# Kernel optimization log

Hardware: AMD Instinct MI355X
Metric: run time of the kernel (lower is better)

Reference implementation:

```python
import jax, jax.numpy as jnp
import numpy as np

B, S, DM, H = 8, 1024, 256, 8
D = DM // H  # 32


def setup_inputs() -> dict:
    key = jax.random.key(0)
    ks = jax.random.split(key, 8)
    xav = (6.0 / (DM + DM)) ** 0.5  # xavier_uniform bound for square Linear
    return {
        "q": jax.random.normal(ks[0], (B, S, DM), jnp.float32),
        "k": jax.random.normal(ks[1], (B, S, DM), jnp.float32),
        "v": jax.random.normal(ks[2], (B, S, DM), jnp.float32),
        "mask": jnp.tril(jnp.ones((1, 1, S, S), jnp.int32)),  # causal: mask==0 is disallowed
        "zero_pad": 1,
        "k_index": 5,
        "Wk": jax.random.uniform(ks[3], (DM, DM), jnp.float32, -xav, xav),
        "bk": jnp.zeros((DM,), jnp.float32),
        "Wv": jax.random.uniform(ks[4], (DM, DM), jnp.float32, -xav, xav),
        "bv": jnp.zeros((DM,), jnp.float32),
        "Wo": jax.random.uniform(ks[5], (DM, DM), jnp.float32, -xav, xav),
        "bo": jnp.zeros((DM,), jnp.float32),
    }


def _attention4sparse_kt(qh, kh, vh, mask, zero_pad, k_index):
    # qh/kh/vh: [B,H,S,D]; mask: [1,1,S,S]
    d = qh.shape[-1]
    scores = jnp.einsum("bhid,bhjd->bhij", qh, kh) / jnp.sqrt(jnp.float32(d))
    scores = jnp.where(mask == 0, jnp.float32(-1e32), scores)
    attn = jax.nn.softmax(scores, axis=-1)  # [B,H,S,S]
    seqlen = attn.shape[2]
    if k_index + 1 < seqlen:
        # per-row k_index-th largest prob as threshold; keep top-k_index entries, re-softmax
        thresh = jax.lax.top_k(attn, k_index)[0][..., -1:]  # [B,H,S,1]
        sparse = jnp.where(attn - thresh >= 0.0, attn, jnp.float32(-1e16))
        resoft = jax.nn.softmax(sparse, axis=-1)
        rows = jnp.arange(seqlen)[None, None, :, None]
        # rows 0..k_index keep the original softmax; later rows use sparsified re-softmax
        attn = jnp.where(rows <= k_index, attn, resoft)
    if zero_pad:
        attn = attn.at[:, :, 0, :].set(0.0)
    out = jnp.einsum("bhij,bhjd->bhid", attn, vh)
    return out, attn


def reference(q, k, v, mask, zero_pad, k_index, Wk, bk, Wv, bv, Wo, bo):
    bs = q.shape[0]
    # key_query_same=True: q and k share k_linear
    kh = (k @ Wk.T + bk).reshape(bs, -1, H, D).transpose(0, 2, 1, 3)
    qh = (q @ Wk.T + bk).reshape(bs, -1, H, D).transpose(0, 2, 1, 3)
    vh = (v @ Wv.T + bv).reshape(bs, -1, H, D).transpose(0, 2, 1, 3)
    out, attn = _attention4sparse_kt(qh, kh, vh, mask, zero_pad, k_index)
    concat = out.transpose(0, 2, 1, 3).reshape(bs, -1, DM)
    output = concat @ Wo.T + bo
    return output, attn
```

## Files before the change

### kernel.cpp

```cpp
#include <hip/hip_runtime.h>
#include <cfloat>
#include <cmath>

#define S_LEN  1024
#define DHEAD  32
#define NHEAD  8
#define DMODEL 256

__global__ __launch_bounds__(256)
void proj_gemm(const float* __restrict__ q, const float* __restrict__ k, const float* __restrict__ v,
               const float* __restrict__ Wk, const float* __restrict__ bk,
               const float* __restrict__ Wv, const float* __restrict__ bv,
               float* __restrict__ qh, float* __restrict__ kh, float* __restrict__ vh)
{
    __shared__ float Xs[128*36];
    __shared__ float Ws_[128*36];
    const int z = blockIdx.z;
    const float* X    = (z==0) ? q  : ((z==1) ? k  : v);
    const float* W    = (z==2) ? Wv : Wk;
    const float* bias = (z==2) ? bv : bk;
    float*       C    = (z==0) ? qh : ((z==1) ? kh : vh);

    const int tid  = threadIdx.x;
    const int row0 = blockIdx.x * 128;
    const int col0 = blockIdx.y * 128;
    const int tx = tid & 15, ty = tid >> 4;
    const int sr = tid >> 1, shf = tid & 1;

    float acc[8][8];
    #pragma unroll
    for (int a = 0; a < 8; ++a)
        #pragma unroll
        for (int b = 0; b < 8; ++b) acc[a][b] = 0.f;

    const int xg = ty & 7;
    const int wg = tx & 7;
    const int swb = (sr >> 3) & 7;

    for (int k0 = 0; k0 < DMODEL; k0 += 32) {
        const float4* xp = (const float4*)(X + (size_t)(row0 + sr) * DMODEL + k0 + shf*16);
        const float4* wp = (const float4*)(W + (size_t)(col0 + sr) * DMODEL + k0 + shf*16);
        float4 xv[4], wv[4];
        #pragma unroll
        for (int q4 = 0; q4 < 4; ++q4) { xv[q4] = xp[q4]; wv[q4] = wp[q4]; }
        if (k0) __syncthreads();
        #pragma unroll
        for (int q4 = 0; q4 < 4; ++q4) {
            const int slot = (shf*4 + q4) ^ swb;
            *(float4*)&Xs [sr*36 + slot*4] = xv[q4];
            *(float4*)&Ws_[sr*36 + slot*4] = wv[q4];
        }
        __syncthreads();
        #pragma unroll
        for (int g = 0; g < 8; ++g) {
            float4 xf[8];
            #pragma unroll
            for (int ri = 0; ri < 8; ++ri)
                xf[ri] = *(const float4*)&Xs[(ty*8+ri)*36 + ((g ^ xg) << 2)];
            #pragma unroll
            for (int ci = 0; ci < 8; ++ci) {
                const float4 wf = *(const float4*)&Ws_[(tx*8+ci)*36 + ((g ^ wg) << 2)];
                #pragma unroll
                for (int ri = 0; ri < 8; ++ri) {
                    acc[ri][ci] += xf[ri].x * wf.x;
                    acc[ri][ci] += xf[ri].y * wf.y;
                    acc[ri][ci] += xf[ri].z * wf.z;
                    acc[ri][ci] += xf[ri].w * wf.w;
                }
            }
        }
    }

    #pragma unroll
    for (int ri = 0; ri < 8; ++ri) {
        const int r = row0 + ty*8 + ri;
        const int bI = r >> 10, s = r & 1023;
        #pragma unroll
        for (int half = 0; half < 2; ++half) {
            const int c = col0 + tx*8 + half*4;
            const float4 bv4 = *(const float4*)(bias + c);
            float4 o;
            o.x = acc[ri][half*4+0] + bv4.x;
            o.y = acc[ri][half*4+1] + bv4.y;
            o.z = acc[ri][half*4+2] + bv4.z;
            o.w = acc[ri][half*4+3] + bv4.w;
            const int h = c >> 5, d0 = c & 31;
            *(float4*)(C + (((size_t)(bI*NHEAD + h))*S_LEN + s)*DHEAD + d0) = o;
        }
    }
}

__global__ __launch_bounds__(256)
void out_gemm(const float* __restrict__ X, const float* __restrict__ W,
              const float* __restrict__ bias, float* __restrict__ C)
{
    __shared__ float Xs[128*36];
    __shared__ float Ws_[64*36];
    const int tid  = threadIdx.x;
    const int row0 = blockIdx.x * 128;
    const int col0 = blockIdx.y * 64;
    const int tx = tid & 15, ty = tid >> 4;
    const int sr = tid >> 1, shf = tid & 1;
    const int wc = tid >> 2, wq = tid & 3;

    float acc[8][4];
    #pragma unroll
    for (int a = 0; a < 8; ++a)
        #pragma unroll
        for (int b = 0; b < 4; ++b) acc[a][b] = 0.f;

    const int xg  = ty & 7;
    const int wg2 = (tx >> 1) & 7;
    const int swbx = (sr >> 3) & 7;
    const int swbw = (wc >> 3) & 7;

    for (int k0 = 0; k0 < DMODEL; k0 += 32) {
        const float4* xp = (const float4*)(X + (size_t)(row0 + sr) * DMODEL + k0 + shf*16);
        const float4* wp = (const float4*)(W + (size_t)(col0 + wc) * DMODEL + k0 + wq*8);
        float4 xv[4], wv[2];
        #pragma unroll
        for (int q4 = 0; q4 < 4; ++q4) xv[q4] = xp[q4];
        #pragma unroll
        for (int q2 = 0; q2 < 2; ++q2) wv[q2] = wp[q2];
        if (k0) __syncthreads();
        #pragma unroll
        for (int q4 = 0; q4 < 4; ++q4) {
            const int slot = (shf*4 + q4) ^ swbx;
            *(float4*)&Xs[sr*36 + slot*4] = xv[q4];
        }
        #pragma unroll
        for (int q2 = 0; q2 < 2; ++q2) {
            const int slot = (wq*2 + q2) ^ swbw;
            *(float4*)&Ws_[wc*36 + slot*4] = wv[q2];
        }
        __syncthreads();
        #pragma unroll
        for (int g = 0; g < 8; ++g) {
            float4 xf[8];
            #pragma unroll
            for (int ri = 0; ri < 8; ++ri)
                xf[ri] = *(const float4*)&Xs[(ty*8+ri)*36 + ((g ^ xg) << 2)];
            #pragma unroll
            for (int ci = 0; ci < 4; ++ci) {
                const float4 wf = *(const float4*)&Ws_[(tx*4+ci)*36 + ((g ^ wg2) << 2)];
                #pragma unroll
                for (int ri = 0; ri < 8; ++ri) {
                    acc[ri][ci] += xf[ri].x * wf.x;
                    acc[ri][ci] += xf[ri].y * wf.y;
                    acc[ri][ci] += xf[ri].z * wf.z;
                    acc[ri][ci] += xf[ri].w * wf.w;
                }
            }
        }
    }

    #pragma unroll
    for (int ri = 0; ri < 8; ++ri) {
        const int r = row0 + ty*8 + ri;
        const int c = col0 + tx*4;
        const float4 bv4 = *(const float4*)(bias + c);
        float4 o;
        o.x = acc[ri][0] + bv4.x; o.y = acc[ri][1] + bv4.y;
        o.z = acc[ri][2] + bv4.z; o.w = acc[ri][3] + bv4.w;
        *(float4*)(C + (size_t)r * DMODEL + c) = o;
    }
}

__device__ __forceinline__ float process_row(
    float (&s)[4][4], const int i, const int l, const int kidx, const int zp,
    const float* __restrict__ vbase, float* __restrict__ arow)
{
    const int vcol = l & 31;
    float m = -FLT_MAX;
    #pragma unroll
    for (int t = 0; t < 4; ++t)
        #pragma unroll
        for (int e = 0; e < 4; ++e) m = fmaxf(m, s[t][e]);
    #pragma unroll
    for (int off = 32; off >= 1; off >>= 1) m = fmaxf(m, __shfl_xor(m, off, 64));

    float e_[4][4]; float Z = 0.f;
    #pragma unroll
    for (int t = 0; t < 4; ++t)
        #pragma unroll
        for (int e = 0; e < 4; ++e) { const float x = expf(s[t][e] - m); e_[t][e] = x; Z += x; }
    #pragma unroll
    for (int off = 32; off >= 1; off >>= 1) Z += __shfl_xor(Z, off, 64);

    float p[4][4];
    #pragma unroll
    for (int t = 0; t < 4; ++t)
        #pragma unroll
        for (int e = 0; e < 4; ++e) p[t][e] = e_[t][e] / Z;

    float tk[8];
    #pragma unroll
    for (int u = 0; u < 8; ++u) tk[u] = -FLT_MAX;
    #pragma unroll
    for (int t = 0; t < 4; ++t)
        #pragma unroll
        for (int e = 0; e < 4; ++e) {
            const float v = p[t][e];
            if (v > tk[7]) {
                float w = v;
                #pragma unroll
                for (int u = 0; u < 8; ++u) {
                    const float mx = fmaxf(tk[u], w);
                    const float mn = fminf(tk[u], w);
                    tk[u] = mx; w = mn;
                }
            }
        }
    float thresh = -FLT_MAX;
    for (int round = 0; round < kidx; ++round) {
        float g = tk[0];
        #pragma unroll
        for (int off = 32; off >= 1; off >>= 1) g = fmaxf(g, __shfl_xor(g, off, 64));
        thresh = g;
        const unsigned long long bb = __ballot(tk[0] == g);
        const int leader = (int)__ffsll(bb) - 1;
        if (l == leader) {
            tk[0]=tk[1]; tk[1]=tk[2]; tk[2]=tk[3]; tk[3]=tk[4];
            tk[4]=tk[5]; tk[5]=tk[6]; tk[6]=tk[7]; tk[7]=-FLT_MAX;
        }
    }

    const bool  sparse = (i > kidx);
    const float pmax   = 1.0f / Z;
    float S2 = 0.f;
    if (sparse) {
        #pragma unroll
        for (int t = 0; t < 4; ++t)
            #pragma unroll
            for (int e = 0; e < 4; ++e)
                if (p[t][e] - thresh >= 0.f) S2 += expf(p[t][e] - pmax);
        #pragma unroll
        for (int off = 32; off >= 1; off >>= 1) S2 += __shfl_xor(S2, off, 64);
    }

    const bool zr = (i == 0) && (zp != 0);
    float w[4][4];
    #pragma unroll
    for (int t = 0; t < 4; ++t)
        #pragma unroll
        for (int e = 0; e < 4; ++e) {
            float ww;
            if (zr)          ww = 0.f;
            else if (!sparse) ww = p[t][e];
            else              ww = (p[t][e] - thresh >= 0.f) ? expf(p[t][e] - pmax) / S2 : 0.f;
            w[t][e] = ww;
        }
    #pragma unroll
    for (int t = 0; t < 4; ++t) {
        float4 f; f.x = w[t][0]; f.y = w[t][1]; f.z = w[t][2]; f.w = w[t][3];
        *(float4*)(arow + t*256 + 4*l) = f;
    }
    float o = 0.f;
    #pragma unroll
    for (int t = 0; t < 4; ++t)
        #pragma unroll
        for (int e = 0; e < 4; ++e) {
            unsigned long long mask = __ballot(w[t][e] != 0.f);
            while (mask) {
                const int src = (int)__ffsll(mask) - 1;
                mask &= mask - 1;
                const float wb = __shfl(w[t][e], src, 64);
                const int j = t*256 + 4*src + e;
                o += wb * vbase[(size_t)j * DHEAD + vcol];
            }
        }
    return o;
}

__global__ __launch_bounds__(512)
void attn_sparse_v2(const float* __restrict__ qh, const float* __restrict__ kh,
                    const float* __restrict__ vh,
                    const int* __restrict__ zp_p, const int* __restrict__ ki_p,
                    float* __restrict__ attn, float* __restrict__ outp)
{
    __shared__ float kT[32*264];
    const int tid = threadIdx.x;
    const int l = tid & 63, w = tid >> 6;
    const int g0 = blockIdx.x;
    const int bh = ((g0 & 7) << 3) + ((g0 >> 3) & 7);
    const int qb = g0 >> 6;
    const int i0 = qb * 16;
    const int iA = i0 + 2*w, iB = iA + 1;
    const int zp = zp_p[0];
    int kidx = ki_p[0];
    if (kidx < 1) kidx = 1;
    if (kidx > 8) kidx = 8;
    const float SCALE = sqrtf((float)DHEAD);

    const float* kb = kh + (size_t)bh * S_LEN * DHEAD;
    const float* vb = vh + (size_t)bh * S_LEN * DHEAD;

    float qa[32], qbr[32];
    {
        const float4* qpA = (const float4*)(qh + ((size_t)bh*S_LEN + iA)*DHEAD);
        const float4* qpB = (const float4*)(qh + ((size_t)bh*S_LEN + iB)*DHEAD);
        #pragma unroll
        for (int t4 = 0; t4 < 8; ++t4) {
            const float4 a = qpA[t4], b = qpB[t4];
            qa [t4*4+0]=a.x; qa [t4*4+1]=a.y; qa [t4*4+2]=a.z; qa [t4*4+3]=a.w;
            qbr[t4*4+0]=b.x; qbr[t4*4+1]=b.y; qbr[t4*4+2]=b.z; qbr[t4*4+3]=b.w;
        }
    }

    float sA[4][4], sB[4][4];
    #pragma unroll
    for (int t = 0; t < 4; ++t)
        #pragma unroll
        for (int e = 0; e < 4; ++e) { sA[t][e] = -FLT_MAX; sB[t][e] = -FLT_MAX; }

    #pragma unroll
    for (int t = 0; t < 4; ++t) {
        if (t*256 <= i0 + 15) {
            if (t > 0) __syncthreads();
            {
                const int jj = tid >> 1, hf = tid & 1;
                const float4* kp = (const float4*)(kb + ((size_t)(t*256 + jj))*DHEAD + hf*16);
                const float4 k0 = kp[0], k1 = kp[1], k2 = kp[2], k3 = kp[3];
                float* cb = &kT[jj];
                const int rb = hf*16;
                cb[(rb+ 0)*264]=k0.x; cb[(rb+ 1)*264]=k0.y; cb[(rb+ 2)*264]=k0.z; cb[(rb+ 3)*264]=k0.w;
                cb[(rb+ 4)*264]=k1.x; cb[(rb+ 5)*264]=k1.y; cb[(rb+ 6)*264]=k1.z; cb[(rb+ 7)*264]=k1.w;
                cb[(rb+ 8)*264]=k2.x; cb[(rb+ 9)*264]=k2.y; cb[(rb+10)*264]=k2.z; cb[(rb+11)*264]=k2.w;
                cb[(rb+12)*264]=k3.x; cb[(rb+13)*264]=k3.y; cb[(rb+14)*264]=k3.z; cb[(rb+15)*264]=k3.w;
            }
            __syncthreads();
            if (t*256 <= iB) {
                float dA[4] = {0.f,0.f,0.f,0.f}, dB[4] = {0.f,0.f,0.f,0.f};
                #pragma unroll
                for (int kk = 0; kk < 32; ++kk) {
                    const float4 kv = *(const float4*)&kT[kk*264 + 4*l];
                    dA[0] += qa[kk]*kv.x; dA[1] += qa[kk]*kv.y;
                    dA[2] += qa[kk]*kv.z; dA[3] += qa[kk]*kv.w;
                    dB[0] += qbr[kk]*kv.x; dB[1] += qbr[kk]*kv.y;
                    dB[2] += qbr[kk]*kv.z; dB[3] += qbr[kk]*kv.w;
                }
                #pragma unroll
                for (int e = 0; e < 4; ++e) {
                    const int j = t*256 + 4*l + e;
                    if (j <= iA) sA[t][e] = dA[e] / SCALE;
                    if (j <= iB) sB[t][e] = dB[e] / SCALE;
                }
            }
        }
    }

    float* arowA = attn + ((size_t)bh*S_LEN + iA)*S_LEN;
    float* arowB = attn + ((size_t)bh*S_LEN + iB)*S_LEN;
    const float oA = process_row(sA, iA, l, kidx, zp, vb, arowA);
    const float oB = process_row(sB, iB, l, kidx, zp, vb, arowB);

    const int srow = iA + (l >> 5);
    const float oval = (l < 32) ? oA : oB;
    outp[((size_t)(bh >> 3)*S_LEN + srow)*DMODEL + (bh & 7)*DHEAD + (l & 31)] = oval;
}

extern "C" void kernel_launch(void* const* d_in, const int* in_sizes, int n_in,
                              void* d_out, int out_size, void* d_ws, size_t ws_size,
                              hipStream_t stream)
{
    (void)in_sizes; (void)n_in; (void)out_size; (void)ws_size;

    const float* q  = (const float*)d_in[0];
    const float* k  = (const float*)d_in[1];
    const float* v  = (const float*)d_in[2];
    const int*   zp = (const int*)d_in[4];
    const int*   ki = (const int*)d_in[5];
    const float* Wk = (const float*)d_in[6];
    const float* bk = (const float*)d_in[7];
    const float* Wv = (const float*)d_in[8];
    const float* bv = (const float*)d_in[9];
    const float* Wo = (const float*)d_in[10];
    const float* bo = (const float*)d_in[11];

    float* out  = (float*)d_out;
    float* attn = (float*)d_out + 2097152;

    float* ws   = (float*)d_ws;
    float* qh   = ws;
    float* kh   = ws + 2097152;
    float* vhp  = ws + 2*2097152;
    float* outp = ws + 3*2097152;

    hipLaunchKernelGGL(proj_gemm, dim3(64, 2, 3), dim3(256), 0, stream,
                       q, k, v, Wk, bk, Wv, bv, qh, kh, vhp);

    hipLaunchKernelGGL(attn_sparse_v2, dim3(4096), dim3(512), 0, stream,
                       qh, kh, vhp, zp, ki, attn, outp);

    hipLaunchKernelGGL(out_gemm, dim3(64, 4), dim3(256), 0, stream,
                       outp, Wo, bo, out);
}
```

Before: 724.9 us.

## Unify projection GEMMs into 128x64 tile, double-buffer K staging, streamline sparse softmax

The projection GEMM now reuses the 128x64 out-GEMM kernel through a template mode, which doubles the block count to improve occupancy at the cost of less data reuse per block. The attention kernel double-buffers the transposed K tile in shared memory, so loading the next chunk overlaps with the dot products and one barrier per chunk is dropped. The softmax/top-k path works on unnormalized exponentials, replaces divisions with reciprocal multiplies, and fuses selection with the re-softmax exponent, adding a tolerance fallback to keep threshold ties consistent. Shared memory per block doubles, which may reduce the number of resident blocks.

```diff
diff --git a/kernel.cpp b/kernel.cpp
--- a/kernel.cpp
+++ b/kernel.cpp
@@ -7,95 +7,25 @@
 #define NHEAD  8
 #define DMODEL 256
 
+template<int MODE>
 __global__ __launch_bounds__(256)
-void proj_gemm(const float* __restrict__ q, const float* __restrict__ k, const float* __restrict__ v,
-               const float* __restrict__ Wk, const float* __restrict__ bk,
-               const float* __restrict__ Wv, const float* __restrict__ bv,
-               float* __restrict__ qh, float* __restrict__ kh, float* __restrict__ vh)
-{
-    __shared__ float Xs[128*36];
-    __shared__ float Ws_[128*36];
-    const int z = blockIdx.z;
-    const float* X    = (z==0) ? q  : ((z==1) ? k  : v);
-    const float* W    = (z==2) ? Wv : Wk;
-    const float* bias = (z==2) ? bv : bk;
-    float*       C    = (z==0) ? qh : ((z==1) ? kh : vh);
-
-    const int tid  = threadIdx.x;
-    const int row0 = blockIdx.x * 128;
-    const int col0 = blockIdx.y * 128;
-    const int tx = tid & 15, ty = tid >> 4;
-    const int sr = tid >> 1, shf = tid & 1;
-
-    float acc[8][8];
-    #pragma unroll
-    for (int a = 0; a < 8; ++a)
-        #pragma unroll
-        for (int b = 0; b < 8; ++b) acc[a][b] = 0.f;
-
-    const int xg = ty & 7;
-    const int wg = tx & 7;
-    const int swb = (sr >> 3) & 7;
-
-    for (int k0 = 0; k0 < DMODEL; k0 += 32) {
-        const float4* xp = (const float4*)(X + (size_t)(row0 + sr) * DMODEL + k0 + shf*16);
-        const float4* wp = (const float4*)(W + (size_t)(col0 + sr) * DMODEL + k0 + shf*16);
-        float4 xv[4], wv[4];
-        #pragma unroll
-        for (int q4 = 0; q4 < 4; ++q4) { xv[q4] = xp[q4]; wv[q4] = wp[q4]; }
-        if (k0) __syncthreads();
-        #pragma unroll
-        for (int q4 = 0; q4 < 4; ++q4) {
-            const int slot = (shf*4 + q4) ^ swb;
-            *(float4*)&Xs [sr*36 + slot*4] = xv[q4];
-            *(float4*)&Ws_[sr*36 + slot*4] = wv[q4];
-        }
-        __syncthreads();
-        #pragma unroll
-        for (int g = 0; g < 8; ++g) {
-            float4 xf[8];
-            #pragma unroll
-            for (int ri = 0; ri < 8; ++ri)
-                xf[ri] = *(const float4*)&Xs[(ty*8+ri)*36 + ((g ^ xg) << 2)];
-            #pragma unroll
-            for (int ci = 0; ci < 8; ++ci) {
-                const float4 wf = *(const float4*)&Ws_[(tx*8+ci)*36 + ((g ^ wg) << 2)];
-                #pragma unroll
-                for (int ri = 0; ri < 8; ++ri) {
-                    acc[ri][ci] += xf[ri].x * wf.x;
-                    acc[ri][ci] += xf[ri].y * wf.y;
-                    acc[ri][ci] += xf[ri].z * wf.z;
-                    acc[ri][ci] += xf[ri].w * wf.w;
-                }
-            }
-        }
-    }
-
-    #pragma unroll
-    for (int ri = 0; ri < 8; ++ri) {
-        const int r = row0 + ty*8 + ri;
-        const int bI = r >> 10, s = r & 1023;
-        #pragma unroll
-        for (int half = 0; half < 2; ++half) {
-            const int c = col0 + tx*8 + half*4;
-            const float4 bv4 = *(const float4*)(bias + c);
-            float4 o;
-            o.x = acc[ri][half*4+0] + bv4.x;
-            o.y = acc[ri][half*4+1] + bv4.y;
-            o.z = acc[ri][half*4+2] + bv4.z;
-            o.w = acc[ri][half*4+3] + bv4.w;
-            const int h = c >> 5, d0 = c & 31;
-            *(float4*)(C + (((size_t)(bI*NHEAD + h))*S_LEN + s)*DHEAD + d0) = o;
-        }
-    }
-}
-
-__global__ __launch_bounds__(256)
-void out_gemm(const float* __restrict__ X, const float* __restrict__ W,
-              const float* __restrict__ bias, float* __restrict__ C)
+void gemm128x64(const float* __restrict__ X0, const float* __restrict__ X1,
+                const float* __restrict__ X2,
+                const float* __restrict__ WA, const float* __restrict__ bA,
+                const float* __restrict__ WB, const float* __restrict__ bB,
+                float* __restrict__ C0, float* __restrict__ C1, float* __restrict__ C2)
 {
     __shared__ float Xs[128*36];
     __shared__ float Ws_[64*36];
+    const float* X; const float* W; const float* bias; float* C;
+    if (MODE == 0) {
+        const int z = blockIdx.z;
+        X    = (z==0) ? X0 : ((z==1) ? X1 : X2);
+        W    = (z==2) ? WB : WA;
+        bias = (z==2) ? bB : bA;
+        C    = (z==0) ? C0 : ((z==1) ? C1 : C2);
+    } else { X = X0; W = WA; bias = bA; C = C0; }
+
     const int tid  = threadIdx.x;
     const int row0 = blockIdx.x * 128;
     const int col0 = blockIdx.y * 64;
@@ -109,8 +39,8 @@
         #pragma unroll
         for (int b = 0; b < 4; ++b) acc[a][b] = 0.f;
 
-    const int xg  = ty & 7;
-    const int wg2 = (tx >> 1) & 7;
+    const int xg   = ty & 7;
+    const int wg2  = (tx >> 1) & 7;
     const int swbx = (sr >> 3) & 7;
     const int swbw = (wc >> 3) & 7;
 
@@ -154,20 +84,26 @@
         }
     }
 
+    const int c = col0 + tx*4;
+    const float4 bv4 = *(const float4*)(bias + c);
     #pragma unroll
     for (int ri = 0; ri < 8; ++ri) {
         const int r = row0 + ty*8 + ri;
-        const int c = col0 + tx*4;
-        const float4 bv4 = *(const float4*)(bias + c);
         float4 o;
         o.x = acc[ri][0] + bv4.x; o.y = acc[ri][1] + bv4.y;
         o.z = acc[ri][2] + bv4.z; o.w = acc[ri][3] + bv4.w;
-        *(float4*)(C + (size_t)r * DMODEL + c) = o;
+        if (MODE == 0) {
+            const int bI = r >> 10, s = r & 1023;
+            const int h = c >> 5, d0 = c & 31;
+            *(float4*)(C + (((size_t)(bI*NHEAD + h))*S_LEN + s)*DHEAD + d0) = o;
+        } else {
+            *(float4*)(C + (size_t)r * DMODEL + c) = o;
+        }
     }
 }
 
-__device__ __forceinline__ float process_row(
-    float (&s)[4][4], const int i, const int l, const int kidx, const int zp,
+__device__ __forceinline__ float process_row_v3(
+    float (&e_)[4][4], const int i, const int l, const int kidx, const int zp,
     const float* __restrict__ vbase, float* __restrict__ arow)
 {
     const int vcol = l & 31;
@@ -175,24 +111,18 @@
     #pragma unroll
     for (int t = 0; t < 4; ++t)
         #pragma unroll
-        for (int e = 0; e < 4; ++e) m = fmaxf(m, s[t][e]);
+        for (int e = 0; e < 4; ++e) m = fmaxf(m, e_[t][e]);
     #pragma unroll
     for (int off = 32; off >= 1; off >>= 1) m = fmaxf(m, __shfl_xor(m, off, 64));
 
-    float e_[4][4]; float Z = 0.f;
-    #pragma unroll
-    for (int t = 0; t < 4; ++t)
-        #pragma unroll
-        for (int e = 0; e < 4; ++e) { const float x = expf(s[t][e] - m); e_[t][e] = x; Z += x; }
+    float Z = 0.f;
+    #pragma unroll
+    for (int t = 0; t < 4; ++t)
+        #pragma unroll
+        for (int e = 0; e < 4; ++e) { const float x = expf(e_[t][e] - m); e_[t][e] = x; Z += x; }
     #pragma unroll
     for (int off = 32; off >= 1; off >>= 1) Z += __shfl_xor(Z, off, 64);
 
-    float p[4][4];
-    #pragma unroll
-    for (int t = 0; t < 4; ++t)
-        #pragma unroll
-        for (int e = 0; e < 4; ++e) p[t][e] = e_[t][e] / Z;
-
     float tk[8];
     #pragma unroll
     for (int u = 0; u < 8; ++u) tk[u] = -FLT_MAX;
@@ -200,7 +130,7 @@
     for (int t = 0; t < 4; ++t)
         #pragma unroll
         for (int e = 0; e < 4; ++e) {
-            const float v = p[t][e];
+            const float v = e_[t][e];
             if (v > tk[7]) {
                 float w = v;
                 #pragma unroll
@@ -211,12 +141,12 @@
                 }
             }
         }
-    float thresh = -FLT_MAX;
+    float te = -FLT_MAX;
     for (int round = 0; round < kidx; ++round) {
         float g = tk[0];
         #pragma unroll
         for (int off = 32; off >= 1; off >>= 1) g = fmaxf(g, __shfl_xor(g, off, 64));
-        thresh = g;
+        te = g;
         const unsigned long long bb = __ballot(tk[0] == g);
         const int leader = (int)__ffsll(bb) - 1;
         if (l == leader) {
@@ -225,46 +155,57 @@
         }
     }
 
+    const float rZ = 1.0f / Z;
     const bool  sparse = (i > kidx);
-    const float pmax   = 1.0f / Z;
-    float S2 = 0.f;
+    const bool  zr = (i == 0) && (zp != 0);
+    float wgt[4][4];
     if (sparse) {
+        const float pth = te / Z;
+        const float tlo = te - te * 2.4e-7f;
+        float S2 = 0.f;
         #pragma unroll
         for (int t = 0; t < 4; ++t)
             #pragma unroll
-            for (int e = 0; e < 4; ++e)
-                if (p[t][e] - thresh >= 0.f) S2 += expf(p[t][e] - pmax);
+            for (int e = 0; e < 4; ++e) {
+                const float ev = e_[t][e];
+                bool sel = (ev >= te);
+                if (!sel && ev >= tlo) {
+                    sel = ((ev / Z) >= pth);
+                }
+                const float x = expf(ev * rZ - rZ);
+                const float xs = sel ? x : 0.f;
+                e_[t][e] = xs;
+                S2 += xs;
+            }
         #pragma unroll
         for (int off = 32; off >= 1; off >>= 1) S2 += __shfl_xor(S2, off, 64);
-    }
-
-    const bool zr = (i == 0) && (zp != 0);
-    float w[4][4];
+        const float rS2 = 1.0f / S2;
+        #pragma unroll
+        for (int t = 0; t < 4; ++t)
+            #pragma unroll
+            for (int e = 0; e < 4; ++e) wgt[t][e] = e_[t][e] * rS2;
+    } else {
+        #pragma unroll
+        for (int t = 0; t < 4; ++t)
+            #pragma unroll
+            for (int e = 0; e < 4; ++e) wgt[t][e] = zr ? 0.f : e_[t][e] * rZ;
+    }
+
+    #pragma unroll
+    for (int t = 0; t < 4; ++t) {
+        float4 f; f.x = wgt[t][0]; f.y = wgt[t][1]; f.z = wgt[t][2]; f.w = wgt[t][3];
+        *(float4*)(arow + t*256 + 4*l) = f;
+    }
+    float o = 0.f;
     #pragma unroll
     for (int t = 0; t < 4; ++t)
         #pragma unroll
         for (int e = 0; e < 4; ++e) {
-            float ww;
-            if (zr)          ww = 0.f;
-            else if (!sparse) ww = p[t][e];
-            else              ww = (p[t][e] - thresh >= 0.f) ? expf(p[t][e] - pmax) / S2 : 0.f;
-            w[t][e] = ww;
-        }
-    #pragma unroll
-    for (int t = 0; t < 4; ++t) {
-        float4 f; f.x = w[t][0]; f.y = w[t][1]; f.z = w[t][2]; f.w = w[t][3];
-        *(float4*)(arow + t*256 + 4*l) = f;
-    }
-    float o = 0.f;
-    #pragma unroll
-    for (int t = 0; t < 4; ++t)
-        #pragma unroll
-        for (int e = 0; e < 4; ++e) {
-            unsigned long long mask = __ballot(w[t][e] != 0.f);
+            unsigned long long mask = __ballot(wgt[t][e] != 0.f);
             while (mask) {
                 const int src = (int)__ffsll(mask) - 1;
                 mask &= mask - 1;
-                const float wb = __shfl(w[t][e], src, 64);
+                const float wb = __shfl(wgt[t][e], src, 64);
                 const int j = t*256 + 4*src + e;
                 o += wb * vbase[(size_t)j * DHEAD + vcol];
             }
@@ -273,12 +214,12 @@
 }
 
 __global__ __launch_bounds__(512)
-void attn_sparse_v2(const float* __restrict__ qh, const float* __restrict__ kh,
+void attn_sparse_v3(const float* __restrict__ qh, const float* __restrict__ kh,
                     const float* __restrict__ vh,
                     const int* __restrict__ zp_p, const int* __restrict__ ki_p,
                     float* __restrict__ attn, float* __restrict__ outp)
 {
-    __shared__ float kT[32*264];
+    __shared__ float kT[2][32*264];
     const int tid = threadIdx.x;
     const int l = tid & 63, w = tid >> 6;
     const int g0 = blockIdx.x;
@@ -290,7 +231,7 @@
     int kidx = ki_p[0];
     if (kidx < 1) kidx = 1;
     if (kidx > 8) kidx = 8;
-    const float SCALE = sqrtf((float)DHEAD);
+    const float INVSCALE = 1.0f / sqrtf((float)DHEAD);
 
     const float* kb = kh + (size_t)bh * S_LEN * DHEAD;
     const float* vb = vh + (size_t)bh * S_LEN * DHEAD;
@@ -313,46 +254,49 @@
         #pragma unroll
         for (int e = 0; e < 4; ++e) { sA[t][e] = -FLT_MAX; sB[t][e] = -FLT_MAX; }
 
+    const int nchunk = ((i0 + 15) >> 8) + 1;
+
+    auto stage = [&](float* buf, int t) {
+        const int jj = tid >> 1, hf = tid & 1;
+        const float4* kp = (const float4*)(kb + ((size_t)(t*256 + jj))*DHEAD + hf*16);
+        const float4 k0 = kp[0], k1 = kp[1], k2 = kp[2], k3 = kp[3];
+        float* cb = buf + jj;
+        const int rb = hf*16;
+        cb[(rb+ 0)*264]=k0.x; cb[(rb+ 1)*264]=k0.y; cb[(rb+ 2)*264]=k0.z; cb[(rb+ 3)*264]=k0.w;
+        cb[(rb+ 4)*264]=k1.x; cb[(rb+ 5)*264]=k1.y; cb[(rb+ 6)*264]=k1.z; cb[(rb+ 7)*264]=k1.w;
+        cb[(rb+ 8)*264]=k2.x; cb[(rb+ 9)*264]=k2.y; cb[(rb+10)*264]=k2.z; cb[(rb+11)*264]=k2.w;
+        cb[(rb+12)*264]=k3.x; cb[(rb+13)*264]=k3.y; cb[(rb+14)*264]=k3.z; cb[(rb+15)*264]=k3.w;
+    };
+
+    stage(kT[0], 0);
     #pragma unroll
     for (int t = 0; t < 4; ++t) {
-        if (t*256 <= i0 + 15) {
-            if (t > 0) __syncthreads();
-            {
-                const int jj = tid >> 1, hf = tid & 1;
-                const float4* kp = (const float4*)(kb + ((size_t)(t*256 + jj))*DHEAD + hf*16);
-                const float4 k0 = kp[0], k1 = kp[1], k2 = kp[2], k3 = kp[3];
-                float* cb = &kT[jj];
-                const int rb = hf*16;
-                cb[(rb+ 0)*264]=k0.x; cb[(rb+ 1)*264]=k0.y; cb[(rb+ 2)*264]=k0.z; cb[(rb+ 3)*264]=k0.w;
-                cb[(rb+ 4)*264]=k1.x; cb[(rb+ 5)*264]=k1.y; cb[(rb+ 6)*264]=k1.z; cb[(rb+ 7)*264]=k1.w;
-                cb[(rb+ 8)*264]=k2.x; cb[(rb+ 9)*264]=k2.y; cb[(rb+10)*264]=k2.z; cb[(rb+11)*264]=k2.w;
-                cb[(rb+12)*264]=k3.x; cb[(rb+13)*264]=k3.y; cb[(rb+14)*264]=k3.z; cb[(rb+15)*264]=k3.w;
-            }
+        if (t < nchunk) {
             __syncthreads();
-            if (t*256 <= iB) {
-                float dA[4] = {0.f,0.f,0.f,0.f}, dB[4] = {0.f,0.f,0.f,0.f};
-                #pragma unroll
-                for (int kk = 0; kk < 32; ++kk) {
-                    const float4 kv = *(const float4*)&kT[kk*264 + 4*l];
-                    dA[0] += qa[kk]*kv.x; dA[1] += qa[kk]*kv.y;
-                    dA[2] += qa[kk]*kv.z; dA[3] += qa[kk]*kv.w;
-                    dB[0] += qbr[kk]*kv.x; dB[1] += qbr[kk]*kv.y;
-                    dB[2] += qbr[kk]*kv.z; dB[3] += qbr[kk]*kv.w;
-                }
-                #pragma unroll
-                for (int e = 0; e < 4; ++e) {
-                    const int j = t*256 + 4*l + e;
-                    if (j <= iA) sA[t][e] = dA[e] / SCALE;
-                    if (j <= iB) sB[t][e] = dB[e] / SCALE;
-                }
+            if (t + 1 < nchunk) stage(kT[(t+1)&1], t+1);
+            const float* buf = kT[t & 1];
+            float dA[4] = {0.f,0.f,0.f,0.f}, dB[4] = {0.f,0.f,0.f,0.f};
+            #pragma unroll
+            for (int kk = 0; kk < 32; ++kk) {
+                const float4 kv = *(const float4*)&buf[kk*264 + 4*l];
+                dA[0] += qa[kk]*kv.x; dA[1] += qa[kk]*kv.y;
+                dA[2] += qa[kk]*kv.z; dA[3] += qa[kk]*kv.w;
+                dB[0] += qbr[kk]*kv.x; dB[1] += qbr[kk]*kv.y;
+                dB[2] += qbr[kk]*kv.z; dB[3] += qbr[kk]*kv.w;
+            }
+            #pragma unroll
+            for (int e = 0; e < 4; ++e) {
+                const int j = t*256 + 4*l + e;
+                if (j <= iA) sA[t][e] = dA[e] * INVSCALE;
+                if (j <= iB) sB[t][e] = dB[e] * INVSCALE;
             }
         }
     }
 
     float* arowA = attn + ((size_t)bh*S_LEN + iA)*S_LEN;
     float* arowB = attn + ((size_t)bh*S_LEN + iB)*S_LEN;
-    const float oA = process_row(sA, iA, l, kidx, zp, vb, arowA);
-    const float oB = process_row(sB, iB, l, kidx, zp, vb, arowB);
+    const float oA = process_row_v3(sA, iA, l, kidx, zp, vb, arowA);
+    const float oB = process_row_v3(sB, iB, l, kidx, zp, vb, arowB);
 
     const int srow = iA + (l >> 5);
     const float oval = (l < 32) ? oA : oB;
@@ -386,12 +330,13 @@
     float* vhp  = ws + 2*2097152;
     float* outp = ws + 3*2097152;
 
-    hipLaunchKernelGGL(proj_gemm, dim3(64, 2, 3), dim3(256), 0, stream,
+    hipLaunchKernelGGL((gemm128x64<0>), dim3(64, 4, 3), dim3(256), 0, stream,
                        q, k, v, Wk, bk, Wv, bv, qh, kh, vhp);
 
-    hipLaunchKernelGGL(attn_sparse_v2, dim3(4096), dim3(512), 0, stream,
+    hipLaunchKernelGGL(attn_sparse_v3, dim3(4096), dim3(512), 0, stream,
                        qh, kh, vhp, zp, ki, attn, outp);
 
-    hipLaunchKernelGGL(out_gemm, dim3(64, 4), dim3(256), 0, stream,
-                       outp, Wo, bo, out);
+    hipLaunchKernelGGL((gemm128x64<1>), dim3(64, 4, 1), dim3(256), 0, stream,
+                       outp, nullptr, nullptr, Wo, bo, nullptr, nullptr,
+                       out, nullptr, nullptr);
 }
```

Result: faster. 676.1 us (-6.7%).
